# Kernel tuning notes

Hardware: AMD Instinct MI355X
Metric: run time of the kernel (lower is better)

## Reference

```python
import jax, jax.numpy as jnp
import numpy as np

B, IN, H, OUT, E = 16384, 256, 512, 32, 8

def setup_inputs() -> dict:
    key = jax.random.key(0)
    ks = jax.random.split(key, 4)
    s1 = 1.0 / np.sqrt(IN); s2 = 1.0 / np.sqrt(H); s3 = 1.0 / np.sqrt(H)
    return {
        "inputs": jax.random.normal(ks[0], (B, IN), dtype=jnp.float32),
        "W1": jax.random.normal(ks[1], (E, IN, H), dtype=jnp.float32) * s1,
        "b1": jnp.zeros((E, H), dtype=jnp.float32),
        "W2": jax.random.normal(ks[2], (E, H, H), dtype=jnp.float32) * s2,
        "b2": jnp.zeros((E, H), dtype=jnp.float32),
        "W3": jax.random.normal(ks[3], (E, H, OUT), dtype=jnp.float32) * s3,
        "b3": jnp.zeros((E, OUT), dtype=jnp.float32),
    }

def reference(inputs, W1, b1, W2, b2, W3, b3):
    # Batched over ensemble dim e: each member is Dense(relu)->Dense(relu)->Dense(linear).
    # inputs: [B, IN]; W1: [E, IN, H]; output: [B, E, OUT] (matches tf.stack(output, axis=1)).
    h = jax.nn.relu(jnp.einsum('bi,eih->beh', inputs, W1) + b1[None, :, :])
    h = jax.nn.relu(jnp.einsum('beh,ehk->bek', h, W2) + b2[None, :, :])
    out = jnp.einsum('beh,eho->beo', h, W3) + b3[None, :, :]
    return out
```

## Files before the change

### kernel.cpp

```cpp
#include <hip/hip_runtime.h>
#include <stdint.h>

typedef short bf16x8 __attribute__((ext_vector_type(8)));
typedef float f32x4  __attribute__((ext_vector_type(4)));

__device__ __forceinline__ uint16_t f2bf(float f) {
    uint32_t u = __float_as_uint(f);
    u += 0x7FFF + ((u >> 16) & 1);
    return (uint16_t)(u >> 16);
}
__device__ __forceinline__ uint32_t pk2bf(float a, float b) {
    return (uint32_t)f2bf(a) | ((uint32_t)f2bf(b) << 16);
}

typedef __attribute__((address_space(1))) const uint32_t gu32;
typedef __attribute__((address_space(3))) uint32_t lu32;
__device__ __forceinline__ void gload16(const void* g, void* l) {
    __builtin_amdgcn_global_load_lds((gu32*)g, (lu32*)l, 16, 0, 0);
}

__global__ __launch_bounds__(256) void prep(
    const float* __restrict__ X,  const float* __restrict__ W1,
    const float* __restrict__ W2, const float* __restrict__ W3,
    uint16_t* __restrict__ xbf, uint16_t* __restrict__ w1t,
    uint16_t* __restrict__ w2t, uint16_t* __restrict__ w3t)
{
    const int b = blockIdx.x, tid = threadIdx.x;
    if (b < 4096) {
        const int i = b * 256 + tid;
        const float4 v = ((const float4*)X)[i];
        ushort4 h;
        h.x = f2bf(v.x); h.y = f2bf(v.y); h.z = f2bf(v.z); h.w = f2bf(v.w);
        ((ushort4*)xbf)[i] = h;
        return;
    }
    __shared__ float t[32][33];
    const int tx = tid & 31, ty = tid >> 5;
    const float* in; uint16_t* out; int R, C, bx, by, e;
    if (b < 5120) {
        const int bb = b - 4096; e = bb >> 7; const int rem = bb & 127;
        bx = rem & 15; by = rem >> 4; R = 256; C = 512; in = W1; out = w1t;
    } else if (b < 7168) {
        const int bb = b - 5120; e = bb >> 8; const int rem = bb & 255;
        bx = rem & 15; by = rem >> 4; R = 512; C = 512; in = W2; out = w2t;
    } else {
        const int bb = b - 7168; e = bb >> 4; bx = 0; by = bb & 15;
        R = 512; C = 32; in = W3; out = w3t;
    }
    const int r0 = by * 32, c0 = bx * 32;
    const float* ine = in + (size_t)e * R * C;
    uint16_t* oute   = out + (size_t)e * R * C;
#pragma unroll
    for (int j = 0; j < 4; ++j)
        t[ty + 8 * j][tx] = ine[(size_t)(r0 + ty + 8 * j) * C + (c0 + tx)];
    __syncthreads();
#pragma unroll
    for (int j = 0; j < 4; ++j) {
        const int orow = c0 + ty + 8 * j;
        const int ocol = r0 + tx;
        oute[(size_t)orow * R + ocol] = f2bf(t[tx][ty + 8 * j]);
    }
}

__global__ __launch_bounds__(1024, 1) void fused128w16(
    const uint16_t* __restrict__ xbf,
    const uint16_t* __restrict__ W1t, const float* __restrict__ b1,
    const uint16_t* __restrict__ W2t, const float* __restrict__ b2,
    const uint16_t* __restrict__ W3t, const float* __restrict__ b3,
    float* __restrict__ out)
{
    extern __shared__ char smem[];
    char* h1buf = smem;
    char* wstg  = smem + 131072;

    const int tid = threadIdx.x, wid = tid >> 6, lane = tid & 63;
    const int kg = lane >> 4, lr = lane & 15;
    const int e   = blockIdx.x;
    const int bm0 = blockIdx.y * 128;
    const int wm = wid >> 2, wn = wid & 3;
    const int rlo = lane >> 3, pslot = lane & 7;
    const int lswz = (pslot ^ rlo) * 8;

    const uint16_t* Xb  = xbf + (size_t)bm0 * 256;
    const uint16_t* W1e = W1t + (size_t)e * 512 * 256;
    const uint16_t* W2e = W2t + (size_t)e * 512 * 512;
    const uint16_t* W3e = W3t + (size_t)e * 32 * 512;

    auto stageW = [&](const uint16_t* We, int K, int cur, int nq, int kt) {
        const int r = wid * 8 + rlo;
        gload16(We + (size_t)(nq * 128 + r) * K + kt * 64 + lswz,
                wstg + cur * 16384 + wid * 1024 + lane * 16);
    };

#pragma unroll
    for (int kt = 0; kt < 4; ++kt) {
        const int r = wid * 8 + rlo;
        gload16(Xb + (size_t)r * 256 + kt * 64 + lswz,
                h1buf + kt * 16384 + wid * 1024 + lane * 16);
    }
    stageW(W1e, 256, 0, 0, 0);
    __syncthreads();

    f32x4 a1[4][2][2];
#pragma unroll
    for (int q = 0; q < 4; ++q)
#pragma unroll
        for (int b = 0; b < 2; ++b)
#pragma unroll
            for (int c = 0; c < 2; ++c) a1[q][b][c] = f32x4{0.f, 0.f, 0.f, 0.f};

#pragma unroll
    for (int p = 0; p < 16; ++p) {
        const int nq = p >> 2, kt = p & 3, cur = p & 1;
        if (p + 1 < 16) stageW(W1e, 256, cur ^ 1, (p + 1) >> 2, (p + 1) & 3);
        asm volatile("" ::: "memory");
        __builtin_amdgcn_s_setprio(1);
#pragma unroll
        for (int kh = 0; kh < 2; ++kh) {
            bf16x8 wf[2], af[2];
#pragma unroll
            for (int c = 0; c < 2; ++c) {
                const int row = wn * 32 + c * 16 + lr;
                wf[c] = *(const bf16x8*)(wstg + cur * 16384 + row * 128 +
                                         (((kh * 4 + kg) ^ (row & 7)) << 4));
            }
#pragma unroll
            for (int b = 0; b < 2; ++b) {
                const int row = wm * 32 + b * 16 + lr;
                af[b] = *(const bf16x8*)(h1buf + kt * 16384 + row * 128 +
                                         (((kh * 4 + kg) ^ (row & 7)) << 4));
            }
#pragma unroll
            for (int b = 0; b < 2; ++b)
#pragma unroll
                for (int c = 0; c < 2; ++c)
                    a1[nq][b][c] = __builtin_amdgcn_mfma_f32_16x16x32_bf16(wf[c], af[b], a1[nq][b][c], 0, 0, 0);
        }
        __builtin_amdgcn_s_setprio(0);
        __syncthreads();
    }

#pragma unroll
    for (int nq = 0; nq < 4; ++nq)
#pragma unroll
        for (int c = 0; c < 2; ++c) {
            const int col = nq * 128 + wn * 32 + c * 16 + kg * 4;
            const float4 bv = *(const float4*)(b1 + e * 512 + col);
#pragma unroll
            for (int b = 0; b < 2; ++b) {
                const float x0 = fmaxf(a1[nq][b][c][0] + bv.x, 0.f);
                const float x1 = fmaxf(a1[nq][b][c][1] + bv.y, 0.f);
                const float x2 = fmaxf(a1[nq][b][c][2] + bv.z, 0.f);
                const float x3 = fmaxf(a1[nq][b][c][3] + bv.w, 0.f);
                uint2 w;
                w.x = pk2bf(x0, x1);
                w.y = pk2bf(x2, x3);
                const int row = wm * 32 + b * 16 + lr;
                *(uint2*)(h1buf + row * 1024 + (((col << 1)) ^ ((row & 7) << 4))) = w;
            }
        }
    __syncthreads();

    const int mf = wid >> 1, of = wid & 1;
    f32x4 o3 = f32x4{0.f, 0.f, 0.f, 0.f};

#pragma unroll
    for (int nq = 0; nq < 4; ++nq) {
        stageW(W2e, 512, 0, nq, 0);
        __syncthreads();

        f32x4 a2[2][2];
#pragma unroll
        for (int b = 0; b < 2; ++b)
#pragma unroll
            for (int c = 0; c < 2; ++c) a2[b][c] = f32x4{0.f, 0.f, 0.f, 0.f};

#pragma unroll
        for (int kt = 0; kt < 8; ++kt) {
            const int cur = kt & 1;
            if (kt + 1 < 8) stageW(W2e, 512, cur ^ 1, nq, kt + 1);
            asm volatile("" ::: "memory");
            __builtin_amdgcn_s_setprio(1);
#pragma unroll
            for (int kh = 0; kh < 2; ++kh) {
                bf16x8 wf[2], af[2];
#pragma unroll
                for (int c = 0; c < 2; ++c) {
                    const int row = wn * 32 + c * 16 + lr;
                    wf[c] = *(const bf16x8*)(wstg + cur * 16384 + row * 128 +
                                             (((kh * 4 + kg) ^ (row & 7)) << 4));
                }
                const int kbyte = kt * 128 + kh * 64 + kg * 16;
#pragma unroll
                for (int b = 0; b < 2; ++b) {
                    const int row = wm * 32 + b * 16 + lr;
                    af[b] = *(const bf16x8*)(h1buf + row * 1024 +
                                             (kbyte ^ ((row & 7) << 4)));
                }
#pragma unroll
                for (int b = 0; b < 2; ++b)
#pragma unroll
                    for (int c = 0; c < 2; ++c)
                        a2[b][c] = __builtin_amdgcn_mfma_f32_16x16x32_bf16(wf[c], af[b], a2[b][c], 0, 0, 0);
            }
            __builtin_amdgcn_s_setprio(0);
            __syncthreads();
        }

#pragma unroll
        for (int c = 0; c < 2; ++c) {
            const int colh = wn * 32 + c * 16 + kg * 4;
            const float4 bv = *(const float4*)(b2 + e * 512 + nq * 128 + colh);
#pragma unroll
            for (int b = 0; b < 2; ++b) {
                const float x0 = fmaxf(a2[b][c][0] + bv.x, 0.f);
                const float x1 = fmaxf(a2[b][c][1] + bv.y, 0.f);
                const float x2 = fmaxf(a2[b][c][2] + bv.z, 0.f);
                const float x3 = fmaxf(a2[b][c][3] + bv.w, 0.f);
                uint2 w;
                w.x = pk2bf(x0, x1);
                w.y = pk2bf(x2, x3);
                const int row = wm * 32 + b * 16 + lr;
                *(uint2*)(wstg + row * 256 + (((colh << 1)) ^ ((row & 7) << 4))) = w;
            }
        }
        __syncthreads();

#pragma unroll
        for (int kcq = 0; kcq < 4; ++kcq) {
            const int row = mf * 16 + lr;
            const bf16x8 hb = *(const bf16x8*)(wstg + row * 256 +
                                               ((kcq * 64 + kg * 16) ^ ((row & 7) << 4)));
            const bf16x8 w3 = *(const bf16x8*)(W3e + (size_t)(of * 16 + lr) * 512 +
                                               nq * 128 + kcq * 32 + kg * 8);
            o3 = __builtin_amdgcn_mfma_f32_16x16x32_bf16(w3, hb, o3, 0, 0, 0);
        }
        __syncthreads();
    }

    {
        const int col = e * 32 + of * 16 + kg * 4;
        const float4 bv = *(const float4*)(b3 + col);
        const int row = bm0 + mf * 16 + lr;
        float4 res;
        res.x = o3[0] + bv.x;
        res.y = o3[1] + bv.y;
        res.z = o3[2] + bv.z;
        res.w = o3[3] + bv.w;
        *(float4*)(out + (size_t)row * 256 + col) = res;
    }
}

extern "C" void kernel_launch(void* const* d_in, const int* in_sizes, int n_in,
                              void* d_out, int out_size, void* d_ws, size_t ws_size,
                              hipStream_t stream) {
    (void)in_sizes; (void)n_in; (void)out_size; (void)ws_size;
    const float* X  = (const float*)d_in[0];
    const float* W1 = (const float*)d_in[1];
    const float* b1 = (const float*)d_in[2];
    const float* W2 = (const float*)d_in[3];
    const float* b2 = (const float*)d_in[4];
    const float* W3 = (const float*)d_in[5];
    const float* b3 = (const float*)d_in[6];
    float* out = (float*)d_out;

    uint16_t* w1t = (uint16_t*)d_ws;
    uint16_t* w2t = w1t + 8 * 256 * 512;
    uint16_t* w3t = w2t + 8 * 512 * 512;
    uint16_t* xbf = w3t + 8 * 512 * 32;

    prep<<<7296, 256, 0, stream>>>(X, W1, W2, W3, xbf, w1t, w2t, w3t);

    (void)hipFuncSetAttribute((const void*)fused128w16,
                              hipFuncAttributeMaxDynamicSharedMemorySize, 163840);
    fused128w16<<<dim3(8, 128), 1024, 163840, stream>>>(xbf, w1t, b1, w2t, b2,
                                                        w3t, b3, out);
}
```

Before: 161.4 us.

## Shrink fused MLP block to 64 rows with 8 waves for more concurrent blocks

Changes the fused kernel from 128-row tiles with 16 waves and 160KB LDS to 64-row tiles with 8 waves, 80KB LDS and 2048 blocks. Each wave now owns one 16-column N fragment per 64-column chunk, so layer loops run over 8 chunks instead of 4. The goal is more blocks resident per CU and better latency hiding and load balance. In exchange, each staged weight tile is reused across half as many rows, doubling weight traffic per output row and the number of barriers.

```diff
diff --git a/kernel.cpp b/kernel.cpp
--- a/kernel.cpp
+++ b/kernel.cpp
@@ -62,7 +62,7 @@
     }
 }
 
-__global__ __launch_bounds__(1024, 1) void fused128w16(
+__global__ __launch_bounds__(512, 4) void fused64s(
     const uint16_t* __restrict__ xbf,
     const uint16_t* __restrict__ W1t, const float* __restrict__ b1,
     const uint16_t* __restrict__ W2t, const float* __restrict__ b2,
@@ -71,12 +71,12 @@
 {
     extern __shared__ char smem[];
     char* h1buf = smem;
-    char* wstg  = smem + 131072;
+    char* wstg  = smem + 65536;
 
     const int tid = threadIdx.x, wid = tid >> 6, lane = tid & 63;
     const int kg = lane >> 4, lr = lane & 15;
     const int e   = blockIdx.x;
-    const int bm0 = blockIdx.y * 128;
+    const int bm0 = blockIdx.y * 64;
     const int wm = wid >> 2, wn = wid & 3;
     const int rlo = lane >> 3, pslot = lane & 7;
     const int lswz = (pslot ^ rlo) * 8;
@@ -86,94 +86,85 @@
     const uint16_t* W2e = W2t + (size_t)e * 512 * 512;
     const uint16_t* W3e = W3t + (size_t)e * 32 * 512;
 
-    auto stageW = [&](const uint16_t* We, int K, int cur, int nq, int kt) {
+    auto stageW = [&](const uint16_t* We, int K, int s, int nq, int kt) {
         const int r = wid * 8 + rlo;
-        gload16(We + (size_t)(nq * 128 + r) * K + kt * 64 + lswz,
-                wstg + cur * 16384 + wid * 1024 + lane * 16);
+        gload16(We + (size_t)(nq * 64 + r) * K + kt * 64 + lswz,
+                wstg + s * 8192 + wid * 1024 + lane * 16);
     };
 
 #pragma unroll
     for (int kt = 0; kt < 4; ++kt) {
         const int r = wid * 8 + rlo;
         gload16(Xb + (size_t)r * 256 + kt * 64 + lswz,
-                h1buf + kt * 16384 + wid * 1024 + lane * 16);
+                h1buf + kt * 8192 + wid * 1024 + lane * 16);
     }
     stageW(W1e, 256, 0, 0, 0);
     __syncthreads();
 
-    f32x4 a1[4][2][2];
-#pragma unroll
-    for (int q = 0; q < 4; ++q)
-#pragma unroll
-        for (int b = 0; b < 2; ++b)
-#pragma unroll
-            for (int c = 0; c < 2; ++c) a1[q][b][c] = f32x4{0.f, 0.f, 0.f, 0.f};
-
-#pragma unroll
-    for (int p = 0; p < 16; ++p) {
+    f32x4 a1[8][2];
+#pragma unroll
+    for (int q = 0; q < 8; ++q)
+#pragma unroll
+        for (int b = 0; b < 2; ++b) a1[q][b] = f32x4{0.f, 0.f, 0.f, 0.f};
+
+#pragma unroll
+    for (int p = 0; p < 32; ++p) {
         const int nq = p >> 2, kt = p & 3, cur = p & 1;
-        if (p + 1 < 16) stageW(W1e, 256, cur ^ 1, (p + 1) >> 2, (p + 1) & 3);
+        if (p + 1 < 32) stageW(W1e, 256, cur ^ 1, (p + 1) >> 2, (p + 1) & 3);
         asm volatile("" ::: "memory");
         __builtin_amdgcn_s_setprio(1);
 #pragma unroll
         for (int kh = 0; kh < 2; ++kh) {
-            bf16x8 wf[2], af[2];
-#pragma unroll
-            for (int c = 0; c < 2; ++c) {
-                const int row = wn * 32 + c * 16 + lr;
-                wf[c] = *(const bf16x8*)(wstg + cur * 16384 + row * 128 +
-                                         (((kh * 4 + kg) ^ (row & 7)) << 4));
+            bf16x8 wf, af[2];
+            {
+                const int row = wn * 16 + lr;
+                wf = *(const bf16x8*)(wstg + cur * 8192 + row * 128 +
+                                      (((kh * 4 + kg) ^ (row & 7)) << 4));
             }
 #pragma unroll
             for (int b = 0; b < 2; ++b) {
                 const int row = wm * 32 + b * 16 + lr;
-                af[b] = *(const bf16x8*)(h1buf + kt * 16384 + row * 128 +
+                af[b] = *(const bf16x8*)(h1buf + kt * 8192 + row * 128 +
                                          (((kh * 4 + kg) ^ (row & 7)) << 4));
             }
 #pragma unroll
             for (int b = 0; b < 2; ++b)
-#pragma unroll
-                for (int c = 0; c < 2; ++c)
-                    a1[nq][b][c] = __builtin_amdgcn_mfma_f32_16x16x32_bf16(wf[c], af[b], a1[nq][b][c], 0, 0, 0);
+                a1[nq][b] = __builtin_amdgcn_mfma_f32_16x16x32_bf16(wf, af[b], a1[nq][b], 0, 0, 0);
         }
         __builtin_amdgcn_s_setprio(0);
         __syncthreads();
     }
 
 #pragma unroll
-    for (int nq = 0; nq < 4; ++nq)
-#pragma unroll
-        for (int c = 0; c < 2; ++c) {
-            const int col = nq * 128 + wn * 32 + c * 16 + kg * 4;
-            const float4 bv = *(const float4*)(b1 + e * 512 + col);
-#pragma unroll
-            for (int b = 0; b < 2; ++b) {
-                const float x0 = fmaxf(a1[nq][b][c][0] + bv.x, 0.f);
-                const float x1 = fmaxf(a1[nq][b][c][1] + bv.y, 0.f);
-                const float x2 = fmaxf(a1[nq][b][c][2] + bv.z, 0.f);
-                const float x3 = fmaxf(a1[nq][b][c][3] + bv.w, 0.f);
-                uint2 w;
-                w.x = pk2bf(x0, x1);
-                w.y = pk2bf(x2, x3);
-                const int row = wm * 32 + b * 16 + lr;
-                *(uint2*)(h1buf + row * 1024 + (((col << 1)) ^ ((row & 7) << 4))) = w;
-            }
-        }
+    for (int nq = 0; nq < 8; ++nq) {
+        const int col = nq * 64 + wn * 16 + kg * 4;
+        const float4 bv = *(const float4*)(b1 + e * 512 + col);
+#pragma unroll
+        for (int b = 0; b < 2; ++b) {
+            const float x0 = fmaxf(a1[nq][b][0] + bv.x, 0.f);
+            const float x1 = fmaxf(a1[nq][b][1] + bv.y, 0.f);
+            const float x2 = fmaxf(a1[nq][b][2] + bv.z, 0.f);
+            const float x3 = fmaxf(a1[nq][b][3] + bv.w, 0.f);
+            uint2 w;
+            w.x = pk2bf(x0, x1);
+            w.y = pk2bf(x2, x3);
+            const int row = wm * 32 + b * 16 + lr;
+            *(uint2*)(h1buf + row * 1024 + (((col << 1)) ^ ((row & 7) << 4))) = w;
+        }
+    }
     __syncthreads();
 
     const int mf = wid >> 1, of = wid & 1;
     f32x4 o3 = f32x4{0.f, 0.f, 0.f, 0.f};
 
 #pragma unroll
-    for (int nq = 0; nq < 4; ++nq) {
+    for (int nq = 0; nq < 8; ++nq) {
         stageW(W2e, 512, 0, nq, 0);
         __syncthreads();
 
-        f32x4 a2[2][2];
-#pragma unroll
-        for (int b = 0; b < 2; ++b)
-#pragma unroll
-            for (int c = 0; c < 2; ++c) a2[b][c] = f32x4{0.f, 0.f, 0.f, 0.f};
+        f32x4 a2[2];
+        a2[0] = f32x4{0.f, 0.f, 0.f, 0.f};
+        a2[1] = f32x4{0.f, 0.f, 0.f, 0.f};
 
 #pragma unroll
         for (int kt = 0; kt < 8; ++kt) {
@@ -183,12 +174,11 @@
             __builtin_amdgcn_s_setprio(1);
 #pragma unroll
             for (int kh = 0; kh < 2; ++kh) {
-                bf16x8 wf[2], af[2];
-#pragma unroll
-                for (int c = 0; c < 2; ++c) {
-                    const int row = wn * 32 + c * 16 + lr;
-                    wf[c] = *(const bf16x8*)(wstg + cur * 16384 + row * 128 +
-                                             (((kh * 4 + kg) ^ (row & 7)) << 4));
+                bf16x8 wf, af[2];
+                {
+                    const int row = wn * 16 + lr;
+                    wf = *(const bf16x8*)(wstg + cur * 8192 + row * 128 +
+                                          (((kh * 4 + kg) ^ (row & 7)) << 4));
                 }
                 const int kbyte = kt * 128 + kh * 64 + kg * 16;
 #pragma unroll
@@ -199,40 +189,37 @@
                 }
 #pragma unroll
                 for (int b = 0; b < 2; ++b)
-#pragma unroll
-                    for (int c = 0; c < 2; ++c)
-                        a2[b][c] = __builtin_amdgcn_mfma_f32_16x16x32_bf16(wf[c], af[b], a2[b][c], 0, 0, 0);
+                    a2[b] = __builtin_amdgcn_mfma_f32_16x16x32_bf16(wf, af[b], a2[b], 0, 0, 0);
             }
             __builtin_amdgcn_s_setprio(0);
             __syncthreads();
         }
 
-#pragma unroll
-        for (int c = 0; c < 2; ++c) {
-            const int colh = wn * 32 + c * 16 + kg * 4;
-            const float4 bv = *(const float4*)(b2 + e * 512 + nq * 128 + colh);
+        {
+            const int colh = wn * 16 + kg * 4;
+            const float4 bv = *(const float4*)(b2 + e * 512 + nq * 64 + colh);
 #pragma unroll
             for (int b = 0; b < 2; ++b) {
-                const float x0 = fmaxf(a2[b][c][0] + bv.x, 0.f);
-                const float x1 = fmaxf(a2[b][c][1] + bv.y, 0.f);
-                const float x2 = fmaxf(a2[b][c][2] + bv.z, 0.f);
-                const float x3 = fmaxf(a2[b][c][3] + bv.w, 0.f);
+                const float x0 = fmaxf(a2[b][0] + bv.x, 0.f);
+                const float x1 = fmaxf(a2[b][1] + bv.y, 0.f);
+                const float x2 = fmaxf(a2[b][2] + bv.z, 0.f);
+                const float x3 = fmaxf(a2[b][3] + bv.w, 0.f);
                 uint2 w;
                 w.x = pk2bf(x0, x1);
                 w.y = pk2bf(x2, x3);
                 const int row = wm * 32 + b * 16 + lr;
-                *(uint2*)(wstg + row * 256 + (((colh << 1)) ^ ((row & 7) << 4))) = w;
-            }
-        }
-        __syncthreads();
-
-#pragma unroll
-        for (int kcq = 0; kcq < 4; ++kcq) {
+                *(uint2*)(wstg + row * 128 + (((colh << 1)) ^ ((row & 7) << 4))) = w;
+            }
+        }
+        __syncthreads();
+
+#pragma unroll
+        for (int kc = 0; kc < 2; ++kc) {
             const int row = mf * 16 + lr;
-            const bf16x8 hb = *(const bf16x8*)(wstg + row * 256 +
-                                               ((kcq * 64 + kg * 16) ^ ((row & 7) << 4)));
+            const bf16x8 hb = *(const bf16x8*)(wstg + row * 128 +
+                                               ((kc * 64 + kg * 16) ^ ((row & 7) << 4)));
             const bf16x8 w3 = *(const bf16x8*)(W3e + (size_t)(of * 16 + lr) * 512 +
-                                               nq * 128 + kcq * 32 + kg * 8);
+                                               nq * 64 + kc * 32 + kg * 8);
             o3 = __builtin_amdgcn_mfma_f32_16x16x32_bf16(w3, hb, o3, 0, 0, 0);
         }
         __syncthreads();
@@ -271,8 +258,8 @@
 
     prep<<<7296, 256, 0, stream>>>(X, W1, W2, W3, xbf, w1t, w2t, w3t);
 
-    (void)hipFuncSetAttribute((const void*)fused128w16,
-                              hipFuncAttributeMaxDynamicSharedMemorySize, 163840);
-    fused128w16<<<dim3(8, 128), 1024, 163840, stream>>>(xbf, w1t, b1, w2t, b2,
-                                                        w3t, b3, out);
-}
+    (void)hipFuncSetAttribute((const void*)fused64s,
+                              hipFuncAttributeMaxDynamicSharedMemorySize, 81920);
+    fused64s<<<dim3(8, 256), 512, 81920, stream>>>(xbf, w1t, b1, w2t, b2,
+                                                   w3t, b3, out);
+}
```

Result: slower. 177.9 us (+10.2%).
